# Optimization experiments

Hardware: AMD Instinct MI355X
Metric: run time of the kernel (lower is better)

## Reference

```python
import jax, jax.numpy as jnp
import numpy as np

N_HEADS = 16
NEG_BIAS = -1000000000.0


def setup_inputs() -> dict:
    key = jax.random.key(0)
    k1, k2, k3, k4 = jax.random.split(key, 4)
    B, S, D = 2, 2048, 1024
    queries = jax.random.normal(k1, (B, S, D), dtype=jnp.float32)
    keys = jax.random.normal(k2, (B, S, D), dtype=jnp.float32)
    values = jax.random.normal(k3, (B, S, D), dtype=jnp.float32)
    mask = jax.random.randint(k4, (B, S, S), 0, 2, dtype=jnp.int32)
    return {"queries": queries, "keys": keys, "values": values, "mask": mask}


def _split_heads(x):
    B, S, D = x.shape
    return x.reshape(B, S, N_HEADS, D // N_HEADS).transpose(0, 2, 1, 3)  # [B,H,S,d]


def reference(queries, keys, values, mask):
    q = _split_heads(queries)   # [B,H,Sq,d]
    k = _split_heads(keys)      # [B,H,Sk,d]
    v = _split_heads(values)    # [B,H,Sk,d]
    d_head = q.shape[-1]
    # scaled dot product similarity
    sim = jnp.einsum('bhqd,bhkd->bhqk', q, k) / jnp.sqrt(jnp.float32(d_head))
    # additive mask (softmax attention function -> non-hadamard)
    bias = NEG_BIAS * (1.0 - mask.astype(sim.dtype))[:, None]  # [B,1,Sq,Sk]
    sim = sim + bias
    # softmax with max-subtraction (numerically stable, as in original)
    weights = jax.nn.softmax(sim, axis=-1)
    out = jnp.einsum('bhqk,bhkd->bhqd', weights, v)  # [B,H,Sq,d]
    B, H, Sq, d = out.shape
    return out.transpose(0, 2, 1, 3).reshape(B, Sq, H * d)
```

## Files before the change

kernel.cpp:

```cpp
#include <hip/hip_runtime.h>

#define S_LEN 2048
#define D_MODEL 1024
#define DH 64
#define BQ 128
#define BK 128
#define ZSCALE 0.18033688f

using short8 = __attribute__((ext_vector_type(8))) short;
using s4v    = __attribute__((ext_vector_type(4))) short;
using f32x4  = __attribute__((ext_vector_type(4))) float;
using u32x4  = __attribute__((ext_vector_type(4))) unsigned int;

#define BMM(a, b, c) __builtin_amdgcn_mfma_f32_16x16x32_bf16((a), (b), (c), 0, 0, 0)
#define LGKM_BAR() do { asm volatile("s_waitcnt lgkmcnt(0)" ::: "memory"); \
                        __builtin_amdgcn_s_barrier(); \
                        __builtin_amdgcn_sched_barrier(0); } while (0)

__device__ __forceinline__ unsigned short f2bf(float x) {
    union { float f; unsigned int u; } c; c.f = x;
    unsigned int u = c.u;
    u += 0x7fffu + ((u >> 16) & 1u);
    return (unsigned short)(u >> 16);
}

__global__ __launch_bounds__(256) void cvt_fused(const float* __restrict__ V,
                                                 const int* __restrict__ M,
                                                 const float* __restrict__ K,
                                                 unsigned short* __restrict__ VT,
                                                 unsigned long long* __restrict__ Mb,
                                                 unsigned short* __restrict__ KB) {
    const int blk = blockIdx.x;
    const int tid = threadIdx.x;
    if (blk < 1024) {
        __shared__ float tsF[64][65];
        const int b  = blk >> 9;
        const int h  = (blk >> 5) & 15;
        const int s0 = (blk & 31) * 64;
        #pragma unroll
        for (int it = 0; it < 2; ++it) {
            int seg = tid + it * 256;
            int s = seg >> 3, d8 = (seg & 7) << 3;
            const float* p = V + (size_t)(b * S_LEN + s0 + s) * D_MODEL + h * DH + d8;
            f32x4 a = *(const f32x4*)p;
            f32x4 c = *(const f32x4*)(p + 4);
            #pragma unroll
            for (int j = 0; j < 4; ++j) { tsF[s][d8 + j] = a[j]; tsF[s][d8 + 4 + j] = c[j]; }
        }
        __syncthreads();
        #pragma unroll
        for (int it = 0; it < 2; ++it) {
            int seg = tid + it * 256;
            int d = seg >> 3, s8 = (seg & 7) << 3;
            short8 w;
            #pragma unroll
            for (int j = 0; j < 8; ++j) w[j] = (short)f2bf(tsF[s8 + j][d]);
            *(short8*)(VT + ((size_t)((b * 16 + h) * 64 + d)) * S_LEN + s0 + s8) = w;
        }
    } else if (blk < 2048) {
        const int pb   = blk - 1024;
        const int wave = tid >> 6, lane = tid & 63;
        const int row  = pb * 4 + wave;
        const int* mp  = M + (size_t)row * S_LEN;
        #pragma unroll 4
        for (int it = 0; it < 32; ++it) {
            int m = mp[it * 64 + lane];
            unsigned long long bal = __ballot(m != 0);
            if (lane == 0) Mb[(size_t)row * 32 + it] = bal;
        }
    } else {
        size_t base = (size_t)(blk - 2048) * 4096;
        #pragma unroll
        for (int it = 0; it < 4; ++it) {
            size_t i = base + ((size_t)(it * 256 + tid)) * 4;
            f32x4 a = *(const f32x4*)(K + i);
            s4v w;
            #pragma unroll
            for (int j = 0; j < 4; ++j) w[j] = (short)f2bf(a[j]);
            *(s4v*)(KB + i) = w;
        }
    }
}

__global__ __launch_bounds__(256) void mha_fwd_v16(
    const float* __restrict__ Q,
    const float* __restrict__ K,
    const unsigned short* __restrict__ KB,
    const unsigned short* __restrict__ VT,
    const unsigned long long* __restrict__ Mb,
    float* __restrict__ O,
    int kbf)
{
    __shared__ alignas(16) unsigned short Ks[2][BK][64];
    __shared__ alignas(16) unsigned short Vt[2][DH][128];

    const int blk0 = blockIdx.x;
    const int blk  = ((blk0 & 7) << 6) | (blk0 >> 3);

    const int b   = blk >> 8;
    const int h   = (blk >> 4) & 15;
    const int qbase = (blk & 15) * BQ;
    const int bh  = b * 16 + h;

    const int tid  = threadIdx.x;
    const int wave = tid >> 6;
    const int lane = tid & 63;
    const int n16  = lane & 15;
    const int quad = lane >> 4;
    const int bq   = quad << 3;
    const int n7   = n16 & 7;

    const int srow = tid >> 3;
    const int prow = (((srow >> 2) & 1) << 4) | (((srow >> 3) & 3) << 2) | (srow & 3);
    const int vrow = tid >> 4;

    const int kwcol = (((tid & 7) ^ (prow & 7)) << 3);
    const int vwcol = (((tid & 15) ^ vrow) << 3);
    const int krc0  = ((quad ^ n7) << 3);
    const int krc1  = krc0 ^ 32;
    int vrc[4];
    #pragma unroll
    for (int kc = 0; kc < 4; ++kc) vrc[kc] = (((kc * 4 + quad) ^ n16) << 3);

    short8 qf[2][2];
    #pragma unroll
    for (int qg = 0; qg < 2; ++qg) {
        const size_t qoff = (size_t)(b * S_LEN + qbase + wave * 32 + qg * 16 + n16) * D_MODEL
                          + h * DH + quad * 8;
        f32x4 a0 = *(const f32x4*)(Q + qoff);
        f32x4 a1 = *(const f32x4*)(Q + qoff + 4);
        f32x4 a2 = *(const f32x4*)(Q + qoff + 32);
        f32x4 a3 = *(const f32x4*)(Q + qoff + 36);
        short8 q0, q1;
        #pragma unroll
        for (int j = 0; j < 4; ++j) {
            q0[j] = (short)f2bf(a0[j] * ZSCALE); q0[4 + j] = (short)f2bf(a1[j] * ZSCALE);
            q1[j] = (short)f2bf(a2[j] * ZSCALE); q1[4 + j] = (short)f2bf(a3[j] * ZSCALE);
        }
        qf[qg][0] = q0; qf[qg][1] = q1;
    }

    const short8 ones = {0x3F80,0x3F80,0x3F80,0x3F80,0x3F80,0x3F80,0x3F80,0x3F80};

    f32x4 o[2][4], o4[2];
    #pragma unroll
    for (int qg = 0; qg < 2; ++qg) {
        #pragma unroll
        for (int dg = 0; dg < 4; ++dg) o[qg][dg] = f32x4{0.f,0.f,0.f,0.f};
        o4[qg] = f32x4{0.f,0.f,0.f,0.f};
    }

    const unsigned long long* mrow[2];
    #pragma unroll
    for (int qg = 0; qg < 2; ++qg)
        mrow[qg] = Mb + (size_t)(b * S_LEN + qbase + wave * 32 + qg * 16 + n16) * 32;

    const size_t kbase = (size_t)(b * S_LEN) * D_MODEL + h * DH;
    const size_t vbase = (size_t)(bh * 64) * S_LEN;

    short8 kaA[4], vaA[4], kaB[4], vaB[4];
    unsigned long long mwA[2][2], mwB[2][2];

    auto LD = [&](int kb2, short8 (&ka)[4], short8 (&va)[4], unsigned long long (&mw)[2][2]) {
        if (kbf) {
            #pragma unroll
            for (int i = 0; i < 4; ++i)
                ka[i] = *(const short8*)(KB + kbase + (size_t)(kb2 + i * 32 + srow) * D_MODEL + ((tid & 7) << 3));
        } else {
            #pragma unroll
            for (int i = 0; i < 4; ++i) {
                const float* kp = K + kbase + (size_t)(kb2 + i * 32 + srow) * D_MODEL + ((tid & 7) << 3);
                f32x4 p0 = *(const f32x4*)kp, p1 = *(const f32x4*)(kp + 4);
                short8 w;
                #pragma unroll
                for (int j = 0; j < 4; ++j) { w[j] = (short)f2bf(p0[j]); w[4 + j] = (short)f2bf(p1[j]); }
                ka[i] = w;
            }
        }
        #pragma unroll
        for (int i = 0; i < 4; ++i)
            va[i] = *(const short8*)(VT + vbase + (size_t)(vrow + 16 * i) * S_LEN + kb2 + ((tid & 15) << 3));
        const int wi = kb2 >> 6;
        #pragma unroll
        for (int qg = 0; qg < 2; ++qg) { mw[qg][0] = mrow[qg][wi]; mw[qg][1] = mrow[qg][wi + 1]; }
    };
    auto MKAM = [&](unsigned long long (&mw)[2][2], unsigned int (&am)[2][4]) {
        #pragma unroll
        for (int qg = 0; qg < 2; ++qg) {
            am[qg][0] = ((unsigned int)mw[qg][0]) >> bq;
            am[qg][1] = ((unsigned int)(mw[qg][0] >> 32)) >> bq;
            am[qg][2] = ((unsigned int)mw[qg][1]) >> bq;
            am[qg][3] = ((unsigned int)(mw[qg][1] >> 32)) >> bq;
        }
    };
    auto QKCT = [&](int pb, int ct, unsigned int (&am)[2][4], u32x4 (&Af)[2][4]) {
        short8 kf0 = *(const short8*)&Ks[pb][ct * 16 + n16][krc0];
        short8 kf1 = *(const short8*)&Ks[pb][ct * 16 + n16][krc1];
        f32x4 sA = {0.f,0.f,0.f,0.f}, sB = sA;
        sA = BMM(kf0, qf[0][0], sA); sA = BMM(kf1, qf[0][1], sA);
        sB = BMM(kf0, qf[1][0], sB); sB = BMM(kf1, qf[1][1], sB);
        unsigned int puA[4], puB[4];
        #pragma unroll
        for (int r = 0; r < 4; ++r) {
            puA[r] = __float_as_uint(__builtin_amdgcn_exp2f(sA[r]));
            puB[r] = __float_as_uint(__builtin_amdgcn_exp2f(sB[r]));
        }
        const int sel = ct >> 1, sb = (ct & 1) * 4, kc = ct >> 1, ub = (ct & 1) * 2;
        unsigned int nibA = (am[0][sel] >> sb) & 0xFu;
        unsigned int nibB = (am[1][sel] >> sb) & 0xFu;
        unsigned int m8A = ((nibA * 0x00204081u) & 0x01010101u) * 0xFFu;
        unsigned int m8B = ((nibB * 0x00204081u) & 0x01010101u) * 0xFFu;
        Af[0][kc][ub + 0] = __builtin_amdgcn_perm(puA[1], puA[0], 0x07060302u)
                          & __builtin_amdgcn_perm(0u, m8A, 0x01010000u);
        Af[0][kc][ub + 1] = __builtin_amdgcn_perm(puA[3], puA[2], 0x07060302u)
                          & __builtin_amdgcn_perm(0u, m8A, 0x03030202u);
        Af[1][kc][ub + 0] = __builtin_amdgcn_perm(puB[1], puB[0], 0x07060302u)
                          & __builtin_amdgcn_perm(0u, m8B, 0x01010000u);
        Af[1][kc][ub + 1] = __builtin_amdgcn_perm(puB[3], puB[2], 0x07060302u)
                          & __builtin_amdgcn_perm(0u, m8B, 0x03030202u);
    };
    auto PVKC = [&](int pb, int kc, u32x4 (&Af)[2][4]) {
        short8 v0 = *(const short8*)&Vt[pb][      n16][vrc[kc]];
        short8 v1 = *(const short8*)&Vt[pb][16 + n16][vrc[kc]];
        short8 v2 = *(const short8*)&Vt[pb][32 + n16][vrc[kc]];
        short8 v3 = *(const short8*)&Vt[pb][48 + n16][vrc[kc]];
        union { u32x4 u; short8 s; } c0, c1;
        c0.u = Af[0][kc]; c1.u = Af[1][kc];
        o[0][0] = BMM(c0.s, v0, o[0][0]); o[0][1] = BMM(c0.s, v1, o[0][1]);
        o[0][2] = BMM(c0.s, v2, o[0][2]); o[0][3] = BMM(c0.s, v3, o[0][3]);
        o4[0]   = BMM(c0.s, ones, o4[0]);
        o[1][0] = BMM(c1.s, v0, o[1][0]); o[1][1] = BMM(c1.s, v1, o[1][1]);
        o[1][2] = BMM(c1.s, v2, o[1][2]); o[1][3] = BMM(c1.s, v3, o[1][3]);
        o4[1]   = BMM(c1.s, ones, o4[1]);
    };
    auto STG = [&](int pb, short8 (&ka)[4], short8 (&va)[4], int i) {
        *(short8*)&Ks[pb][prow + 32 * i][kwcol] = ka[i];
        *(short8*)&Vt[pb][vrow + 16 * i][vwcol] = va[i];
    };
    auto BODY = [&](int pb, unsigned long long (&mwC)[2][2],
                    int ldkb, short8 (&lka)[4], short8 (&lva)[4],
                    unsigned long long (&lmw)[2][2], bool doLoad,
                    short8 (&ska)[4], short8 (&sva)[4], bool doStage) {
        unsigned int am[2][4]; MKAM(mwC, am);
        if (doLoad) LD(ldkb, lka, lva, lmw);
        u32x4 Af[2][4];
        __builtin_amdgcn_s_setprio(1);
        QKCT(pb, 0, am, Af); QKCT(pb, 1, am, Af); PVKC(pb, 0, Af);
        if (doStage) STG(pb ^ 1, ska, sva, 0);
        QKCT(pb, 2, am, Af); QKCT(pb, 3, am, Af); PVKC(pb, 1, Af);
        if (doStage) STG(pb ^ 1, ska, sva, 1);
        QKCT(pb, 4, am, Af); QKCT(pb, 5, am, Af); PVKC(pb, 2, Af);
        if (doStage) STG(pb ^ 1, ska, sva, 2);
        QKCT(pb, 6, am, Af); QKCT(pb, 7, am, Af); PVKC(pb, 3, Af);
        if (doStage) STG(pb ^ 1, ska, sva, 3);
        __builtin_amdgcn_s_setprio(0);
    };

    LD(0, kaA, vaA, mwA);
    #pragma unroll
    for (int i = 0; i < 4; ++i) STG(0, kaA, vaA, i);
    LD(BK, kaB, vaB, mwB);
    LGKM_BAR();

    for (int it = 0; it < 7; ++it) {
        BODY(0, mwA, (2 * it + 2) * BK, kaA, vaA, mwA, true, kaB, vaB, true);
        LGKM_BAR();
        BODY(1, mwB, (2 * it + 3) * BK, kaB, vaB, mwB, true, kaA, vaA, true);
        LGKM_BAR();
    }
    BODY(0, mwA, 0, kaA, vaA, mwA, false, kaB, vaB, true);
    LGKM_BAR();
    BODY(1, mwB, 0, kaB, vaB, mwB, false, kaA, vaA, false);

    #pragma unroll
    for (int qg = 0; qg < 2; ++qg) {
        #pragma unroll
        for (int r = 0; r < 4; ++r) {
            float rl = 1.f / o4[qg][r];
            size_t row = (size_t)(b * S_LEN + qbase + wave * 32 + qg * 16 + quad * 4 + r);
            float* op = O + row * D_MODEL + h * DH + n16;
            op[0]  = o[qg][0][r] * rl;
            op[16] = o[qg][1][r] * rl;
            op[32] = o[qg][2][r] * rl;
            op[48] = o[qg][3][r] * rl;
        }
    }
}

extern "C" void kernel_launch(void* const* d_in, const int* in_sizes, int n_in,
                              void* d_out, int out_size, void* d_ws, size_t ws_size,
                              hipStream_t stream) {
    const float* Q = (const float*)d_in[0];
    const float* K = (const float*)d_in[1];
    const float* V = (const float*)d_in[2];
    const int*   M = (const int*)d_in[3];
    float*       O = (float*)d_out;

    const size_t NEL = (size_t)2 * S_LEN * D_MODEL;
    const size_t VT_BYTES = NEL * sizeof(unsigned short);
    const size_t KB_BYTES = NEL * sizeof(unsigned short);
    const size_t MB_BYTES = (size_t)2 * S_LEN * 32 * 8;

    if (ws_size >= VT_BYTES + KB_BYTES + MB_BYTES) {
        unsigned short* VT = (unsigned short*)d_ws;
        unsigned short* KB = (unsigned short*)((char*)d_ws + VT_BYTES);
        unsigned long long* Mb = (unsigned long long*)((char*)d_ws + VT_BYTES + KB_BYTES);
        hipLaunchKernelGGL(cvt_fused, dim3(3072), dim3(256), 0, stream, V, M, K, VT, Mb, KB);
        hipLaunchKernelGGL(mha_fwd_v16, dim3(512), dim3(256), 0, stream,
                           Q, K, KB, VT, Mb, O, 1);
    } else {
        unsigned short* VT = (unsigned short*)d_ws;
        unsigned long long* Mb = (unsigned long long*)((char*)d_ws + VT_BYTES);
        hipLaunchKernelGGL(cvt_fused, dim3(2048), dim3(256), 0, stream, V, M, K, VT, Mb, (unsigned short*)0);
        hipLaunchKernelGGL(mha_fwd_v16, dim3(512), dim3(256), 0, stream,
                           Q, K, (const unsigned short*)0, VT, Mb, O, 0);
    }
}
```

Baseline: 171.5 us.

## Stage K/V tiles via direct global-to-LDS loads and restructure double buffer

Replaces the register-staged K and V tile loads (global to VGPR, then ds_write) with buffer/global_load_lds instructions that write straight into the swizzled shared-memory tiles. The address swizzle is moved into the per-lane global addresses. The prefetch is issued at the start of each compute phase, and the barrier now waits on vmcnt as well as lgkmcnt. The QK/PV interleave within a tile is also reordered. This removes register pressure and the ds_write instructions, but the full vmcnt wait at each barrier may expose load latency that the old register pipeline hid.

```diff
diff --git a/kernel.cpp b/kernel.cpp
--- a/kernel.cpp
+++ b/kernel.cpp
@@ -13,9 +13,12 @@
 using u32x4  = __attribute__((ext_vector_type(4))) unsigned int;
 
 #define BMM(a, b, c) __builtin_amdgcn_mfma_f32_16x16x32_bf16((a), (b), (c), 0, 0, 0)
-#define LGKM_BAR() do { asm volatile("s_waitcnt lgkmcnt(0)" ::: "memory"); \
+#define FULL_BAR() do { asm volatile("s_waitcnt vmcnt(0) lgkmcnt(0)" ::: "memory"); \
                         __builtin_amdgcn_s_barrier(); \
                         __builtin_amdgcn_sched_barrier(0); } while (0)
+
+typedef const __attribute__((address_space(1))) unsigned int* gas1_t;
+typedef __attribute__((address_space(3))) unsigned int* las3_t;
 
 __device__ __forceinline__ unsigned short f2bf(float x) {
     union { float f; unsigned int u; } c; c.f = x;
@@ -82,7 +85,7 @@
     }
 }
 
-__global__ __launch_bounds__(256) void mha_fwd_v16(
+__global__ __launch_bounds__(256) void mha_fwd_v17(
     const float* __restrict__ Q,
     const float* __restrict__ K,
     const unsigned short* __restrict__ KB,
@@ -113,14 +116,17 @@
     const int srow = tid >> 3;
     const int prow = (((srow >> 2) & 1) << 4) | (((srow >> 3) & 3) << 2) | (srow & 3);
     const int vrow = tid >> 4;
-
     const int kwcol = (((tid & 7) ^ (prow & 7)) << 3);
     const int vwcol = (((tid & 15) ^ vrow) << 3);
+
     const int krc0  = ((quad ^ n7) << 3);
     const int krc1  = krc0 ^ 32;
     int vrc[4];
     #pragma unroll
     for (int kc = 0; kc < 4; ++kc) vrc[kc] = (((kc * 4 + quad) ^ n16) << 3);
+
+    const int kpr  = wave * 32 + (lane >> 3);
+    const int vpr  = wave * 16 + (lane >> 4);
 
     short8 qf[2][2];
     #pragma unroll
@@ -158,14 +164,32 @@
     const size_t kbase = (size_t)(b * S_LEN) * D_MODEL + h * DH;
     const size_t vbase = (size_t)(bh * 64) * S_LEN;
 
-    short8 kaA[4], vaA[4], kaB[4], vaB[4];
     unsigned long long mwA[2][2], mwB[2][2];
 
-    auto LD = [&](int kb2, short8 (&ka)[4], short8 (&va)[4], unsigned long long (&mw)[2][2]) {
+    auto STAGE = [&](int pb, int kb2) {
         if (kbf) {
             #pragma unroll
-            for (int i = 0; i < 4; ++i)
-                ka[i] = *(const short8*)(KB + kbase + (size_t)(kb2 + i * 32 + srow) * D_MODEL + ((tid & 7) << 3));
+            for (int c = 0; c < 4; ++c) {
+                const int pr  = kpr + c * 8;
+                const int prl = pr & 31;
+                const int sr  = (((prl >> 3) & 1) << 4) | (((prl >> 2) & 1) << 3)
+                              | (((prl >> 4) & 1) << 2) | (prl & 3);
+                const int lg  = (lane & 7) ^ (prl & 7);
+                const unsigned short* gp = KB + kbase
+                    + (size_t)(kb2 + (pr >> 5) * 32 + sr) * D_MODEL + lg * 8;
+                __builtin_amdgcn_global_load_lds(
+                    (gas1_t)(const void*)gp,
+                    (las3_t)(void*)&Ks[pb][wave * 32 + c * 8][0], 16, 0, 0);
+            }
+            #pragma unroll
+            for (int c = 0; c < 4; ++c) {
+                const int r  = vpr + c * 4;
+                const int lg = (lane & 15) ^ (r & 15);
+                const unsigned short* gp = VT + vbase + (size_t)r * S_LEN + kb2 + lg * 8;
+                __builtin_amdgcn_global_load_lds(
+                    (gas1_t)(const void*)gp,
+                    (las3_t)(void*)&Vt[pb][wave * 16 + c * 4][0], 16, 0, 0);
+            }
         } else {
             #pragma unroll
             for (int i = 0; i < 4; ++i) {
@@ -174,12 +198,13 @@
                 short8 w;
                 #pragma unroll
                 for (int j = 0; j < 4; ++j) { w[j] = (short)f2bf(p0[j]); w[4 + j] = (short)f2bf(p1[j]); }
-                ka[i] = w;
+                *(short8*)&Ks[pb][prow + 32 * i][kwcol] = w;
+                short8 v = *(const short8*)(VT + vbase + (size_t)(vrow + 16 * i) * S_LEN + kb2 + ((tid & 15) << 3));
+                *(short8*)&Vt[pb][vrow + 16 * i][vwcol] = v;
             }
         }
-        #pragma unroll
-        for (int i = 0; i < 4; ++i)
-            va[i] = *(const short8*)(VT + vbase + (size_t)(vrow + 16 * i) * S_LEN + kb2 + ((tid & 15) << 3));
+    };
+    auto LDM = [&](int kb2, unsigned long long (&mw)[2][2]) {
         const int wi = kb2 >> 6;
         #pragma unroll
         for (int qg = 0; qg < 2; ++qg) { mw[qg][0] = mrow[qg][wi]; mw[qg][1] = mrow[qg][wi + 1]; }
@@ -193,84 +218,81 @@
             am[qg][3] = ((unsigned int)(mw[qg][1] >> 32)) >> bq;
         }
     };
-    auto QKCT = [&](int pb, int ct, unsigned int (&am)[2][4], u32x4 (&Af)[2][4]) {
-        short8 kf0 = *(const short8*)&Ks[pb][ct * 16 + n16][krc0];
-        short8 kf1 = *(const short8*)&Ks[pb][ct * 16 + n16][krc1];
-        f32x4 sA = {0.f,0.f,0.f,0.f}, sB = sA;
-        sA = BMM(kf0, qf[0][0], sA); sA = BMM(kf1, qf[0][1], sA);
-        sB = BMM(kf0, qf[1][0], sB); sB = BMM(kf1, qf[1][1], sB);
-        unsigned int puA[4], puB[4];
-        #pragma unroll
-        for (int r = 0; r < 4; ++r) {
-            puA[r] = __float_as_uint(__builtin_amdgcn_exp2f(sA[r]));
-            puB[r] = __float_as_uint(__builtin_amdgcn_exp2f(sB[r]));
-        }
-        const int sel = ct >> 1, sb = (ct & 1) * 4, kc = ct >> 1, ub = (ct & 1) * 2;
-        unsigned int nibA = (am[0][sel] >> sb) & 0xFu;
-        unsigned int nibB = (am[1][sel] >> sb) & 0xFu;
-        unsigned int m8A = ((nibA * 0x00204081u) & 0x01010101u) * 0xFFu;
-        unsigned int m8B = ((nibB * 0x00204081u) & 0x01010101u) * 0xFFu;
-        Af[0][kc][ub + 0] = __builtin_amdgcn_perm(puA[1], puA[0], 0x07060302u)
-                          & __builtin_amdgcn_perm(0u, m8A, 0x01010000u);
-        Af[0][kc][ub + 1] = __builtin_amdgcn_perm(puA[3], puA[2], 0x07060302u)
-                          & __builtin_amdgcn_perm(0u, m8A, 0x03030202u);
-        Af[1][kc][ub + 0] = __builtin_amdgcn_perm(puB[1], puB[0], 0x07060302u)
-                          & __builtin_amdgcn_perm(0u, m8B, 0x01010000u);
-        Af[1][kc][ub + 1] = __builtin_amdgcn_perm(puB[3], puB[2], 0x07060302u)
-                          & __builtin_amdgcn_perm(0u, m8B, 0x03030202u);
-    };
-    auto PVKC = [&](int pb, int kc, u32x4 (&Af)[2][4]) {
-        short8 v0 = *(const short8*)&Vt[pb][      n16][vrc[kc]];
-        short8 v1 = *(const short8*)&Vt[pb][16 + n16][vrc[kc]];
-        short8 v2 = *(const short8*)&Vt[pb][32 + n16][vrc[kc]];
-        short8 v3 = *(const short8*)&Vt[pb][48 + n16][vrc[kc]];
-        union { u32x4 u; short8 s; } c0, c1;
-        c0.u = Af[0][kc]; c1.u = Af[1][kc];
-        o[0][0] = BMM(c0.s, v0, o[0][0]); o[0][1] = BMM(c0.s, v1, o[0][1]);
-        o[0][2] = BMM(c0.s, v2, o[0][2]); o[0][3] = BMM(c0.s, v3, o[0][3]);
-        o4[0]   = BMM(c0.s, ones, o4[0]);
-        o[1][0] = BMM(c1.s, v0, o[1][0]); o[1][1] = BMM(c1.s, v1, o[1][1]);
-        o[1][2] = BMM(c1.s, v2, o[1][2]); o[1][3] = BMM(c1.s, v3, o[1][3]);
-        o4[1]   = BMM(c1.s, ones, o4[1]);
-    };
-    auto STG = [&](int pb, short8 (&ka)[4], short8 (&va)[4], int i) {
-        *(short8*)&Ks[pb][prow + 32 * i][kwcol] = ka[i];
-        *(short8*)&Vt[pb][vrow + 16 * i][vwcol] = va[i];
-    };
-    auto BODY = [&](int pb, unsigned long long (&mwC)[2][2],
-                    int ldkb, short8 (&lka)[4], short8 (&lva)[4],
-                    unsigned long long (&lmw)[2][2], bool doLoad,
-                    short8 (&ska)[4], short8 (&sva)[4], bool doStage) {
-        unsigned int am[2][4]; MKAM(mwC, am);
-        if (doLoad) LD(ldkb, lka, lva, lmw);
+    auto COMPUTE = [&](int pb, unsigned int (&am)[2][4]) {
         u32x4 Af[2][4];
+        auto QKCT = [&](int ct) {
+            short8 kf0 = *(const short8*)&Ks[pb][ct * 16 + n16][krc0];
+            short8 kf1 = *(const short8*)&Ks[pb][ct * 16 + n16][krc1];
+            f32x4 sA = {0.f,0.f,0.f,0.f}, sB = sA;
+            sA = BMM(kf0, qf[0][0], sA); sA = BMM(kf1, qf[0][1], sA);
+            sB = BMM(kf0, qf[1][0], sB); sB = BMM(kf1, qf[1][1], sB);
+            unsigned int puA[4], puB[4];
+            #pragma unroll
+            for (int r = 0; r < 4; ++r) {
+                puA[r] = __float_as_uint(__builtin_amdgcn_exp2f(sA[r]));
+                puB[r] = __float_as_uint(__builtin_amdgcn_exp2f(sB[r]));
+            }
+            const int sel = ct >> 1, sb = (ct & 1) * 4, kc = ct >> 1, ub = (ct & 1) * 2;
+            unsigned int nibA = (am[0][sel] >> sb) & 0xFu;
+            unsigned int nibB = (am[1][sel] >> sb) & 0xFu;
+            unsigned int m8A = ((nibA * 0x00204081u) & 0x01010101u) * 0xFFu;
+            unsigned int m8B = ((nibB * 0x00204081u) & 0x01010101u) * 0xFFu;
+            Af[0][kc][ub + 0] = __builtin_amdgcn_perm(puA[1], puA[0], 0x07060302u)
+                              & __builtin_amdgcn_perm(0u, m8A, 0x01010000u);
+            Af[0][kc][ub + 1] = __builtin_amdgcn_perm(puA[3], puA[2], 0x07060302u)
+                              & __builtin_amdgcn_perm(0u, m8A, 0x03030202u);
+            Af[1][kc][ub + 0] = __builtin_amdgcn_perm(puB[1], puB[0], 0x07060302u)
+                              & __builtin_amdgcn_perm(0u, m8B, 0x01010000u);
+            Af[1][kc][ub + 1] = __builtin_amdgcn_perm(puB[3], puB[2], 0x07060302u)
+                              & __builtin_amdgcn_perm(0u, m8B, 0x03030202u);
+        };
+        auto PVKC = [&](int kc) {
+            short8 v0 = *(const short8*)&Vt[pb][      n16][vrc[kc]];
+            short8 v1 = *(const short8*)&Vt[pb][16 + n16][vrc[kc]];
+            short8 v2 = *(const short8*)&Vt[pb][32 + n16][vrc[kc]];
+            short8 v3 = *(const short8*)&Vt[pb][48 + n16][vrc[kc]];
+            union { u32x4 u; short8 s; } c0, c1;
+            c0.u = Af[0][kc]; c1.u = Af[1][kc];
+            o[0][0] = BMM(c0.s, v0, o[0][0]); o[0][1] = BMM(c0.s, v1, o[0][1]);
+            o[0][2] = BMM(c0.s, v2, o[0][2]); o[0][3] = BMM(c0.s, v3, o[0][3]);
+            o4[0]   = BMM(c0.s, ones, o4[0]);
+            o[1][0] = BMM(c1.s, v0, o[1][0]); o[1][1] = BMM(c1.s, v1, o[1][1]);
+            o[1][2] = BMM(c1.s, v2, o[1][2]); o[1][3] = BMM(c1.s, v3, o[1][3]);
+            o4[1]   = BMM(c1.s, ones, o4[1]);
+        };
         __builtin_amdgcn_s_setprio(1);
-        QKCT(pb, 0, am, Af); QKCT(pb, 1, am, Af); PVKC(pb, 0, Af);
-        if (doStage) STG(pb ^ 1, ska, sva, 0);
-        QKCT(pb, 2, am, Af); QKCT(pb, 3, am, Af); PVKC(pb, 1, Af);
-        if (doStage) STG(pb ^ 1, ska, sva, 1);
-        QKCT(pb, 4, am, Af); QKCT(pb, 5, am, Af); PVKC(pb, 2, Af);
-        if (doStage) STG(pb ^ 1, ska, sva, 2);
-        QKCT(pb, 6, am, Af); QKCT(pb, 7, am, Af); PVKC(pb, 3, Af);
-        if (doStage) STG(pb ^ 1, ska, sva, 3);
+        QKCT(0); QKCT(1); QKCT(2);
+        PVKC(0);
+        QKCT(3); QKCT(4);
+        PVKC(1);
+        QKCT(5); QKCT(6);
+        PVKC(2);
+        QKCT(7);
+        PVKC(3);
         __builtin_amdgcn_s_setprio(0);
     };
 
-    LD(0, kaA, vaA, mwA);
-    #pragma unroll
-    for (int i = 0; i < 4; ++i) STG(0, kaA, vaA, i);
-    LD(BK, kaB, vaB, mwB);
-    LGKM_BAR();
-
-    for (int it = 0; it < 7; ++it) {
-        BODY(0, mwA, (2 * it + 2) * BK, kaA, vaA, mwA, true, kaB, vaB, true);
-        LGKM_BAR();
-        BODY(1, mwB, (2 * it + 3) * BK, kaB, vaB, mwB, true, kaA, vaA, true);
-        LGKM_BAR();
-    }
-    BODY(0, mwA, 0, kaA, vaA, mwA, false, kaB, vaB, true);
-    LGKM_BAR();
-    BODY(1, mwB, 0, kaB, vaB, mwB, false, kaA, vaA, false);
+    STAGE(0, 0);
+    LDM(0, mwA);
+    FULL_BAR();
+
+    for (int it = 0; it < 8; ++it) {
+        {
+            const int kn = (2 * it + 1) * BK;
+            STAGE(1, kn); LDM(kn, mwB);
+            unsigned int am[2][4]; MKAM(mwA, am);
+            COMPUTE(0, am);
+            FULL_BAR();
+        }
+        {
+            const int kn = (2 * it + 2) * BK;
+            const bool more = kn < S_LEN;
+            if (more) { STAGE(0, kn); LDM(kn, mwA); }
+            unsigned int am[2][4]; MKAM(mwB, am);
+            COMPUTE(1, am);
+            if (more) FULL_BAR();
+        }
+    }
 
     #pragma unroll
     for (int qg = 0; qg < 2; ++qg) {
@@ -306,13 +328,13 @@
         unsigned short* KB = (unsigned short*)((char*)d_ws + VT_BYTES);
         unsigned long long* Mb = (unsigned long long*)((char*)d_ws + VT_BYTES + KB_BYTES);
         hipLaunchKernelGGL(cvt_fused, dim3(3072), dim3(256), 0, stream, V, M, K, VT, Mb, KB);
-        hipLaunchKernelGGL(mha_fwd_v16, dim3(512), dim3(256), 0, stream,
+        hipLaunchKernelGGL(mha_fwd_v17, dim3(512), dim3(256), 0, stream,
                            Q, K, KB, VT, Mb, O, 1);
     } else {
         unsigned short* VT = (unsigned short*)d_ws;
         unsigned long long* Mb = (unsigned long long*)((char*)d_ws + VT_BYTES);
         hipLaunchKernelGGL(cvt_fused, dim3(2048), dim3(256), 0, stream, V, M, K, VT, Mb, (unsigned short*)0);
-        hipLaunchKernelGGL(mha_fwd_v16, dim3(512), dim3(256), 0, stream,
+        hipLaunchKernelGGL(mha_fwd_v17, dim3(512), dim3(256), 0, stream,
                            Q, K, (const unsigned short*)0, VT, Mb, O, 0);
     }
 }
```

New measurement: 171.5 us. No clear change (-0.0%).
